# Optimization experiments

Measured on AMD Instinct MI355X. Metric: run time of the kernel, lower is better.

The kernel has to match this reference:

```python
import jax, jax.numpy as jnp
import numpy as np

VOCAB = 50265
HIDDEN = 768
NUM_LABELS = 2
B, S = 2, 4096


def setup_inputs() -> dict:
    key = jax.random.key(0)
    k1, k2, k3, k4 = jax.random.split(key, 4)
    # near-one-hot / soft distribution over vocab per token (positive values)
    embedding = jax.random.uniform(k1, (B, S, VOCAB), dtype=jnp.float32)
    attention_masks = jnp.ones((B, S), dtype=jnp.int32)
    # nn.Linear(vocab, hidden, bias=False): weight shape (hidden, vocab)
    W_embed = jax.random.normal(k2, (HIDDEN, VOCAB), dtype=jnp.float32) * 0.02
    token_mask = jnp.ones((VOCAB,), dtype=jnp.float32)
    W_cls = jax.random.normal(k3, (NUM_LABELS, HIDDEN), dtype=jnp.float32) * 0.02
    b_cls = jax.random.normal(k4, (NUM_LABELS,), dtype=jnp.float32) * 0.02
    return {"embedding": embedding, "attention_masks": attention_masks,
            "W_embed": W_embed, "token_mask": token_mask,
            "W_cls": W_cls, "b_cls": b_cls}


def reference(embedding, attention_masks, W_embed, token_mask, W_cls, b_cls):
    # norm_data=True: normalize each token's vocab distribution to sum 1
    normalized = embedding / jnp.sum(embedding, axis=-1, keepdims=True)
    # masked one-hot -> dense GEMM with embedding weight: (B,S,V) @ (V,H)
    emb = jnp.einsum('bsv,hv->bsh', normalized * token_mask, W_embed)
    # NOTE: pretrained Longformer body (self.bert) is an external pretrained
    # module; the kernel-relevant math (one-hot GEMM + classifier head) is
    # reproduced here. Classifier applied to the hidden states.
    logits = jnp.einsum('bsh,lh->bsl', emb, W_cls) + b_cls
    return logits
```

## Files before the change

### kernel.cpp

```cpp
#include <hip/hip_runtime.h>
#include <stdint.h>

typedef float vfloat4 __attribute__((ext_vector_type(4)));

constexpr int CHUNK = 4096;
constexpr int TG    = 16;
constexpr int VT    = 2048;
constexpr int MAXNG = 24;

__global__ __launch_bounds__(256) void fuse_partial_kernel(
    const float* __restrict__ Wemb,
    const float* __restrict__ Wcls,
    float* __restrict__ part,
    const int V, const int Vp, const int H, const int NG, const int NVT)
{
    __shared__ float sW0[1024];
    __shared__ float sW1[1024];
    for (int i = threadIdx.x; i < H; i += 256) { sW0[i] = Wcls[i]; sW1[i] = Wcls[H + i]; }
    __syncthreads();

    const int vt = blockIdx.x % NVT;
    const int g  = blockIdx.x / NVT;
    const int HS = (H + NG - 1) / NG;
    const int h0 = g * HS;
    const int h1 = min(H, h0 + HS);
    const int v  = vt * VT + (int)threadIdx.x * 8;

    float a0[8], a1[8];
    #pragma unroll
    for (int k = 0; k < 8; ++k) { a0[k] = 0.f; a1[k] = 0.f; }

    if (v + 8 <= V) {
        for (int h = h0; h < h1; ++h) {
            const float* p = Wemb + (size_t)h * (size_t)V + v;
            vfloat4 x0, x1;
            __builtin_memcpy(&x0, p,     16);
            __builtin_memcpy(&x1, p + 4, 16);
            const float w0 = sW0[h], w1 = sW1[h];
            a0[0] = fmaf(w0, x0.x, a0[0]);
            a0[1] = fmaf(w0, x0.y, a0[1]);
            a0[2] = fmaf(w0, x0.z, a0[2]);
            a0[3] = fmaf(w0, x0.w, a0[3]);
            a0[4] = fmaf(w0, x1.x, a0[4]);
            a0[5] = fmaf(w0, x1.y, a0[5]);
            a0[6] = fmaf(w0, x1.z, a0[6]);
            a0[7] = fmaf(w0, x1.w, a0[7]);
            a1[0] = fmaf(w1, x0.x, a1[0]);
            a1[1] = fmaf(w1, x0.y, a1[1]);
            a1[2] = fmaf(w1, x0.z, a1[2]);
            a1[3] = fmaf(w1, x0.w, a1[3]);
            a1[4] = fmaf(w1, x1.x, a1[4]);
            a1[5] = fmaf(w1, x1.y, a1[5]);
            a1[6] = fmaf(w1, x1.z, a1[6]);
            a1[7] = fmaf(w1, x1.w, a1[7]);
        }
        float* p0 = part + (size_t)g * 2 * (size_t)Vp + v;
        float* p1 = p0 + Vp;
        vfloat4 s00 = {a0[0], a0[1], a0[2], a0[3]};
        vfloat4 s01 = {a0[4], a0[5], a0[6], a0[7]};
        vfloat4 s10 = {a1[0], a1[1], a1[2], a1[3]};
        vfloat4 s11 = {a1[4], a1[5], a1[6], a1[7]};
        *(vfloat4*)(p0)     = s00;
        *(vfloat4*)(p0 + 4) = s01;
        *(vfloat4*)(p1)     = s10;
        *(vfloat4*)(p1 + 4) = s11;
    } else if (v < V) {
        for (int h = h0; h < h1; ++h) {
            const float w0 = sW0[h], w1 = sW1[h];
            const float* p = Wemb + (size_t)h * (size_t)V;
            #pragma unroll
            for (int k = 0; k < 8; ++k) {
                if (v + k < V) {
                    float x = p[v + k];
                    a0[k] = fmaf(w0, x, a0[k]);
                    a1[k] = fmaf(w1, x, a1[k]);
                }
            }
        }
        float* p0 = part + (size_t)g * 2 * (size_t)Vp;
        #pragma unroll
        for (int k = 0; k < 8; ++k) {
            if (v + k < V) { p0[v + k] = a0[k]; p0[Vp + v + k] = a1[k]; }
        }
    }
}

__global__ __launch_bounds__(256) void fuse_reduce_kernel(
    const float* __restrict__ part,
    const float* __restrict__ tmask,
    float2* __restrict__ wf2,
    const int V, const int Vp, const int NG)
{
    const int v = blockIdx.x * 256 + threadIdx.x;
    if (v >= V) return;
    float s0 = 0.f, s1 = 0.f;
    for (int g = 0; g < NG; ++g) {
        const float* p0 = part + (size_t)g * 2 * (size_t)Vp;
        s0 += p0[v];
        s1 += p0[Vp + v];
    }
    const float m = tmask[v];
    wf2[v] = make_float2(s0 * m, s1 * m);
}

__global__ __launch_bounds__(256) void fuse_weights_kernel(
    const float* __restrict__ Wemb,
    const float* __restrict__ tmask,
    const float* __restrict__ Wcls,
    float2* __restrict__ wf2,
    int V, int H)
{
    __shared__ float sW0[1024];
    __shared__ float sW1[1024];
    __shared__ float part[4][64][2];

    for (int i = threadIdx.x; i < H; i += blockDim.x) {
        sW0[i] = Wcls[i];
        sW1[i] = Wcls[H + i];
    }
    __syncthreads();

    const int vl = threadIdx.x & 63;
    const int hg = threadIdx.x >> 6;
    const int v  = blockIdx.x * 64 + vl;

    float a0 = 0.f, a1 = 0.f;
    if (v < V) {
        for (int h = hg; h < H; h += 4) {
            float w = Wemb[(size_t)h * (size_t)V + v];
            a0 = fmaf(w, sW0[h], a0);
            a1 = fmaf(w, sW1[h], a1);
        }
    }
    part[hg][vl][0] = a0;
    part[hg][vl][1] = a1;
    __syncthreads();

    if (hg == 0 && v < V) {
        float r0 = (part[0][vl][0] + part[1][vl][0]) + (part[2][vl][0] + part[3][vl][0]);
        float r1 = (part[0][vl][1] + part[1][vl][1]) + (part[2][vl][1] + part[3][vl][1]);
        float m = tmask[v];
        wf2[v] = make_float2(r0 * m, r1 * m);
    }
}

__global__ __launch_bounds__(256) void partial_kernel(
    const float* __restrict__ emb,
    const float2* __restrict__ wf2,
    float4* __restrict__ part,
    const int V, const int T, const int NC)
{
    __shared__ float lw0[CHUNK];
    __shared__ float lw1[CHUNK];
    __shared__ float red[4][TG][3];

    const int c    = blockIdx.x % NC;
    const int g    = blockIdx.x / NC;
    const int v0   = c * CHUNK;
    const int clen = min(CHUNK, V - v0);
    const int tid  = threadIdx.x;

    for (int i = tid; i < clen; i += 256) {
        float2 w = wf2[v0 + i];
        lw0[i] = w.x;
        lw1[i] = w.y;
    }
    __syncthreads();

    const int t0 = g * TG;
    float sA[TG], dA0[TG], dA1[TG];

    if (clen == CHUNK) {
        #pragma unroll
        for (int tk = 0; tk < TG; ++tk) {
            const float* rp = emb + (size_t)(t0 + tk) * (size_t)V + v0;
            float s = 0.f, d0 = 0.f, d1 = 0.f;
            #pragma unroll
            for (int jj = 0; jj < CHUNK / 1024; ++jj) {
                const int v4 = (tid + jj * 256) << 2;
                vfloat4 ev;
                __builtin_memcpy(&ev, rp + v4, 16);
                const vfloat4 w0 = *(const vfloat4*)(lw0 + v4);
                const vfloat4 w1 = *(const vfloat4*)(lw1 + v4);
                s += (ev.x + ev.y) + (ev.z + ev.w);
                d0 = fmaf(ev.x, w0.x, d0);
                d0 = fmaf(ev.y, w0.y, d0);
                d0 = fmaf(ev.z, w0.z, d0);
                d0 = fmaf(ev.w, w0.w, d0);
                d1 = fmaf(ev.x, w1.x, d1);
                d1 = fmaf(ev.y, w1.y, d1);
                d1 = fmaf(ev.z, w1.z, d1);
                d1 = fmaf(ev.w, w1.w, d1);
            }
            sA[tk] = s; dA0[tk] = d0; dA1[tk] = d1;
        }
    } else {
        const int nb4 = clen >> 2;
        const int rem = clen & 3;
        #pragma unroll
        for (int tk = 0; tk < TG; ++tk) {
            const float* rp = emb + (size_t)(t0 + tk) * (size_t)V + v0;
            float s = 0.f, d0 = 0.f, d1 = 0.f;
            for (int j = tid; j < nb4; j += 256) {
                const int v4 = j << 2;
                vfloat4 ev;
                __builtin_memcpy(&ev, rp + v4, 16);
                const vfloat4 w0 = *(const vfloat4*)(lw0 + v4);
                const vfloat4 w1 = *(const vfloat4*)(lw1 + v4);
                s += (ev.x + ev.y) + (ev.z + ev.w);
                d0 = fmaf(ev.x, w0.x, d0);
                d0 = fmaf(ev.y, w0.y, d0);
                d0 = fmaf(ev.z, w0.z, d0);
                d0 = fmaf(ev.w, w0.w, d0);
                d1 = fmaf(ev.x, w1.x, d1);
                d1 = fmaf(ev.y, w1.y, d1);
                d1 = fmaf(ev.z, w1.z, d1);
                d1 = fmaf(ev.w, w1.w, d1);
            }
            if (tid < rem) {
                const int v = (nb4 << 2) + tid;
                float e = rp[v];
                s += e;
                d0 = fmaf(e, lw0[v], d0);
                d1 = fmaf(e, lw1[v], d1);
            }
            sA[tk] = s; dA0[tk] = d0; dA1[tk] = d1;
        }
    }

    #pragma unroll
    for (int tk = 0; tk < TG; ++tk) {
        float s = sA[tk], d0 = dA0[tk], d1 = dA1[tk];
        #pragma unroll
        for (int off = 32; off > 0; off >>= 1) {
            s  += __shfl_xor(s,  off);
            d0 += __shfl_xor(d0, off);
            d1 += __shfl_xor(d1, off);
        }
        if ((tid & 63) == 0) {
            const int w = tid >> 6;
            red[w][tk][0] = s; red[w][tk][1] = d0; red[w][tk][2] = d1;
        }
    }
    __syncthreads();

    if (tid < TG) {
        float S  = (red[0][tid][0] + red[1][tid][0]) + (red[2][tid][0] + red[3][tid][0]);
        float D0 = (red[0][tid][1] + red[1][tid][1]) + (red[2][tid][1] + red[3][tid][1]);
        float D1 = (red[0][tid][2] + red[1][tid][2]) + (red[2][tid][2] + red[3][tid][2]);
        part[(size_t)c * T + (t0 + tid)] = make_float4(S, D0, D1, 0.f);
    }
}

__global__ __launch_bounds__(256) void finalize_kernel(
    const float4* __restrict__ part,
    const float* __restrict__ bcls,
    float2* __restrict__ out,
    const int T, const int NC)
{
    const int t = blockIdx.x * 256 + threadIdx.x;
    if (t >= T) return;
    float S = 0.f, D0 = 0.f, D1 = 0.f;
    for (int c = 0; c < NC; ++c) {
        float4 p = part[(size_t)c * T + t];
        S += p.x; D0 += p.y; D1 += p.z;
    }
    out[t] = make_float2(D0 / S + bcls[0], D1 / S + bcls[1]);
}

extern "C" void kernel_launch(void* const* d_in, const int* in_sizes, int n_in,
                              void* d_out, int out_size, void* d_ws, size_t ws_size,
                              hipStream_t stream) {
    const float* emb   = (const float*)d_in[0];
    const float* Wemb  = (const float*)d_in[2];
    const float* tmask = (const float*)d_in[3];
    const float* Wcls  = (const float*)d_in[4];
    const float* bcls  = (const float*)d_in[5];

    const int V  = in_sizes[3];
    const int T  = in_sizes[1];
    const int H  = in_sizes[2] / V;
    const int NC = (V + CHUNK - 1) / CHUNK;
    const int Vp = (V + 7) & ~7;

    float2* wf2 = (float2*)d_ws;
    const size_t wf2_b   = (((size_t)V * 8) + 255) & ~(size_t)255;
    const size_t k2p_b   = (((size_t)NC * T * 16) + 255) & ~(size_t)255;
    float4* k2part = (float4*)((char*)d_ws + wf2_b);
    const size_t off_k1p = wf2_b + k2p_b;
    float*  k1part = (float*)((char*)d_ws + off_k1p);

    const size_t per_g = (size_t)2 * Vp * 4;
    int NG = 0;
    if (ws_size > off_k1p) NG = (int)((ws_size - off_k1p) / per_g);
    if (NG > MAXNG) NG = MAXNG;

    if (NG >= 2) {
        const int NVT = (V + VT - 1) / VT;
        fuse_partial_kernel<<<NVT * NG, 256, 0, stream>>>(Wemb, Wcls, k1part, V, Vp, H, NG, NVT);
        fuse_reduce_kernel<<<(V + 255) / 256, 256, 0, stream>>>(k1part, tmask, wf2, V, Vp, NG);
    } else {
        const int blocks1 = (V + 63) / 64;
        fuse_weights_kernel<<<blocks1, 256, 0, stream>>>(Wemb, tmask, Wcls, wf2, V, H);
    }

    const int blocks2 = NC * (T / TG);
    partial_kernel<<<blocks2, 256, 0, stream>>>(emb, wf2, k2part, V, T, NC);

    const int blocks3 = (T + 255) / 256;
    finalize_kernel<<<blocks3, 256, 0, stream>>>(k2part, bcls, (float2*)d_out, T, NC);
}
```

Before: 377.4 us.

## Align token-row loads per residue and keep fused weights in registers

The partial kernel now assigns each block tokens sharing the same row alignment residue (t mod 4). It shifts the chunk start by a per-residue offset so the 16-byte loads of each embedding row are aligned, and handles the few leading elements separately. The fused classifier weights are loaded straight into registers instead of staged through LDS, which drops the shared-memory fill and its barrier. The first fuse kernel also switches from 8 contiguous floats per thread to a 256-stride coalesced pattern. The cost is more index arithmetic and a more complex tail path, with the tail now reading weights from global memory.

```diff
diff --git a/kernel.cpp b/kernel.cpp
--- a/kernel.cpp
+++ b/kernel.cpp
@@ -24,63 +24,45 @@
     const int HS = (H + NG - 1) / NG;
     const int h0 = g * HS;
     const int h1 = min(H, h0 + HS);
-    const int v  = vt * VT + (int)threadIdx.x * 8;
+    const int base = vt * VT + (int)threadIdx.x;
 
     float a0[8], a1[8];
     #pragma unroll
-    for (int k = 0; k < 8; ++k) { a0[k] = 0.f; a1[k] = 0.f; }
-
-    if (v + 8 <= V) {
+    for (int j = 0; j < 8; ++j) { a0[j] = 0.f; a1[j] = 0.f; }
+
+    if ((vt + 1) * VT <= V) {
         for (int h = h0; h < h1; ++h) {
-            const float* p = Wemb + (size_t)h * (size_t)V + v;
-            vfloat4 x0, x1;
-            __builtin_memcpy(&x0, p,     16);
-            __builtin_memcpy(&x1, p + 4, 16);
+            const float* p = Wemb + (size_t)h * (size_t)V + base;
             const float w0 = sW0[h], w1 = sW1[h];
-            a0[0] = fmaf(w0, x0.x, a0[0]);
-            a0[1] = fmaf(w0, x0.y, a0[1]);
-            a0[2] = fmaf(w0, x0.z, a0[2]);
-            a0[3] = fmaf(w0, x0.w, a0[3]);
-            a0[4] = fmaf(w0, x1.x, a0[4]);
-            a0[5] = fmaf(w0, x1.y, a0[5]);
-            a0[6] = fmaf(w0, x1.z, a0[6]);
-            a0[7] = fmaf(w0, x1.w, a0[7]);
-            a1[0] = fmaf(w1, x0.x, a1[0]);
-            a1[1] = fmaf(w1, x0.y, a1[1]);
-            a1[2] = fmaf(w1, x0.z, a1[2]);
-            a1[3] = fmaf(w1, x0.w, a1[3]);
-            a1[4] = fmaf(w1, x1.x, a1[4]);
-            a1[5] = fmaf(w1, x1.y, a1[5]);
-            a1[6] = fmaf(w1, x1.z, a1[6]);
-            a1[7] = fmaf(w1, x1.w, a1[7]);
-        }
-        float* p0 = part + (size_t)g * 2 * (size_t)Vp + v;
-        float* p1 = p0 + Vp;
-        vfloat4 s00 = {a0[0], a0[1], a0[2], a0[3]};
-        vfloat4 s01 = {a0[4], a0[5], a0[6], a0[7]};
-        vfloat4 s10 = {a1[0], a1[1], a1[2], a1[3]};
-        vfloat4 s11 = {a1[4], a1[5], a1[6], a1[7]};
-        *(vfloat4*)(p0)     = s00;
-        *(vfloat4*)(p0 + 4) = s01;
-        *(vfloat4*)(p1)     = s10;
-        *(vfloat4*)(p1 + 4) = s11;
-    } else if (v < V) {
+            #pragma unroll
+            for (int j = 0; j < 8; ++j) {
+                float x = p[j * 256];
+                a0[j] = fmaf(w0, x, a0[j]);
+                a1[j] = fmaf(w1, x, a1[j]);
+            }
+        }
+        float* o0 = part + (size_t)g * 2 * (size_t)Vp + base;
+        #pragma unroll
+        for (int j = 0; j < 8; ++j) { o0[j * 256] = a0[j]; o0[Vp + j * 256] = a1[j]; }
+    } else {
         for (int h = h0; h < h1; ++h) {
+            const float* p = Wemb + (size_t)h * (size_t)V;
             const float w0 = sW0[h], w1 = sW1[h];
-            const float* p = Wemb + (size_t)h * (size_t)V;
-            #pragma unroll
-            for (int k = 0; k < 8; ++k) {
-                if (v + k < V) {
-                    float x = p[v + k];
-                    a0[k] = fmaf(w0, x, a0[k]);
-                    a1[k] = fmaf(w1, x, a1[k]);
+            #pragma unroll
+            for (int j = 0; j < 8; ++j) {
+                const int v = base + j * 256;
+                if (v < V) {
+                    float x = p[v];
+                    a0[j] = fmaf(w0, x, a0[j]);
+                    a1[j] = fmaf(w1, x, a1[j]);
                 }
             }
         }
-        float* p0 = part + (size_t)g * 2 * (size_t)Vp;
+        float* o0 = part + (size_t)g * 2 * (size_t)Vp;
         #pragma unroll
-        for (int k = 0; k < 8; ++k) {
-            if (v + k < V) { p0[v + k] = a0[k]; p0[Vp + v + k] = a1[k]; }
+        for (int j = 0; j < 8; ++j) {
+            const int v = base + j * 256;
+            if (v < V) { o0[v] = a0[j]; o0[Vp + v] = a1[j]; }
         }
     }
 }
@@ -104,11 +86,8 @@
 }
 
 __global__ __launch_bounds__(256) void fuse_weights_kernel(
-    const float* __restrict__ Wemb,
-    const float* __restrict__ tmask,
-    const float* __restrict__ Wcls,
-    float2* __restrict__ wf2,
-    int V, int H)
+    const float* __restrict__ Wemb, const float* __restrict__ tmask,
+    const float* __restrict__ Wcls, float2* __restrict__ wf2, int V, int H)
 {
     __shared__ float sW0[1024];
     __shared__ float sW1[1024];
@@ -150,113 +129,114 @@
     float4* __restrict__ part,
     const int V, const int T, const int NC)
 {
-    __shared__ float lw0[CHUNK];
-    __shared__ float lw1[CHUNK];
     __shared__ float red[4][TG][3];
 
-    const int c    = blockIdx.x % NC;
-    const int g    = blockIdx.x / NC;
-    const int v0   = c * CHUNK;
-    const int clen = min(CHUNK, V - v0);
-    const int tid  = threadIdx.x;
-
-    for (int i = tid; i < clen; i += 256) {
-        float2 w = wf2[v0 + i];
-        lw0[i] = w.x;
-        lw1[i] = w.y;
-    }
-    __syncthreads();
-
-    const int t0 = g * TG;
-    float sA[TG], dA0[TG], dA1[TG];
-
-    if (clen == CHUNK) {
+    const int tid = threadIdx.x;
+    const int c   = blockIdx.x % NC;
+    const int g   = blockIdx.x / NC;
+    const int r   = g & 3;
+    const int q   = g >> 2;
+    const int h   = (4 - r) & 3;
+    const int wstart = h + c * CHUNK;
+    const int wlen   = min(CHUNK, V - wstart);
+    const int voff   = tid << 2;
+    const int wv     = tid >> 6;
+
+    if (wlen == CHUNK) {
+        vfloat4 w0v[4], w1v[4];
         #pragma unroll
+        for (int jj = 0; jj < 4; ++jj) {
+            float2 f[4];
+            __builtin_memcpy(f, wf2 + (wstart + voff + jj * 1024), 32);
+            w0v[jj] = (vfloat4){f[0].x, f[1].x, f[2].x, f[3].x};
+            w1v[jj] = (vfloat4){f[0].y, f[1].y, f[2].y, f[3].y};
+        }
+
         for (int tk = 0; tk < TG; ++tk) {
-            const float* rp = emb + (size_t)(t0 + tk) * (size_t)V + v0;
+            const int t = r + 64 * q + 4 * tk;
+            const float* rp = emb + (size_t)t * (size_t)V + wstart;
             float s = 0.f, d0 = 0.f, d1 = 0.f;
             #pragma unroll
-            for (int jj = 0; jj < CHUNK / 1024; ++jj) {
-                const int v4 = (tid + jj * 256) << 2;
-                vfloat4 ev;
-                __builtin_memcpy(&ev, rp + v4, 16);
-                const vfloat4 w0 = *(const vfloat4*)(lw0 + v4);
-                const vfloat4 w1 = *(const vfloat4*)(lw1 + v4);
+            for (int jj = 0; jj < 4; ++jj) {
+                const vfloat4 ev = *(const vfloat4*)(rp + voff + jj * 1024);
                 s += (ev.x + ev.y) + (ev.z + ev.w);
-                d0 = fmaf(ev.x, w0.x, d0);
-                d0 = fmaf(ev.y, w0.y, d0);
-                d0 = fmaf(ev.z, w0.z, d0);
-                d0 = fmaf(ev.w, w0.w, d0);
-                d1 = fmaf(ev.x, w1.x, d1);
-                d1 = fmaf(ev.y, w1.y, d1);
-                d1 = fmaf(ev.z, w1.z, d1);
-                d1 = fmaf(ev.w, w1.w, d1);
-            }
-            sA[tk] = s; dA0[tk] = d0; dA1[tk] = d1;
+                d0 = fmaf(ev.x, w0v[jj].x, d0);
+                d0 = fmaf(ev.y, w0v[jj].y, d0);
+                d0 = fmaf(ev.z, w0v[jj].z, d0);
+                d0 = fmaf(ev.w, w0v[jj].w, d0);
+                d1 = fmaf(ev.x, w1v[jj].x, d1);
+                d1 = fmaf(ev.y, w1v[jj].y, d1);
+                d1 = fmaf(ev.z, w1v[jj].z, d1);
+                d1 = fmaf(ev.w, w1v[jj].w, d1);
+            }
+            if (c == 0 && tid < h) {
+                const float e = emb[(size_t)t * (size_t)V + tid];
+                const float2 w = wf2[tid];
+                s += e; d0 = fmaf(e, w.x, d0); d1 = fmaf(e, w.y, d1);
+            }
+            #pragma unroll
+            for (int off = 32; off > 0; off >>= 1) {
+                s  += __shfl_xor(s,  off);
+                d0 += __shfl_xor(d0, off);
+                d1 += __shfl_xor(d1, off);
+            }
+            if ((tid & 63) == 0) {
+                red[wv][tk][0] = s; red[wv][tk][1] = d0; red[wv][tk][2] = d1;
+            }
         }
     } else {
-        const int nb4 = clen >> 2;
-        const int rem = clen & 3;
-        #pragma unroll
+        const int nb4 = wlen >> 2;
+        const int rem = wlen & 3;
         for (int tk = 0; tk < TG; ++tk) {
-            const float* rp = emb + (size_t)(t0 + tk) * (size_t)V + v0;
+            const int t = r + 64 * q + 4 * tk;
+            const float* rp = emb + (size_t)t * (size_t)V + wstart;
             float s = 0.f, d0 = 0.f, d1 = 0.f;
             for (int j = tid; j < nb4; j += 256) {
                 const int v4 = j << 2;
-                vfloat4 ev;
-                __builtin_memcpy(&ev, rp + v4, 16);
-                const vfloat4 w0 = *(const vfloat4*)(lw0 + v4);
-                const vfloat4 w1 = *(const vfloat4*)(lw1 + v4);
+                const vfloat4 ev = *(const vfloat4*)(rp + v4);
+                float2 f[4];
+                __builtin_memcpy(f, wf2 + (wstart + v4), 32);
                 s += (ev.x + ev.y) + (ev.z + ev.w);
-                d0 = fmaf(ev.x, w0.x, d0);
-                d0 = fmaf(ev.y, w0.y, d0);
-                d0 = fmaf(ev.z, w0.z, d0);
-                d0 = fmaf(ev.w, w0.w, d0);
-                d1 = fmaf(ev.x, w1.x, d1);
-                d1 = fmaf(ev.y, w1.y, d1);
-                d1 = fmaf(ev.z, w1.z, d1);
-                d1 = fmaf(ev.w, w1.w, d1);
+                d0 = fmaf(ev.x, f[0].x, d0);
+                d0 = fmaf(ev.y, f[1].x, d0);
+                d0 = fmaf(ev.z, f[2].x, d0);
+                d0 = fmaf(ev.w, f[3].x, d0);
+                d1 = fmaf(ev.x, f[0].y, d1);
+                d1 = fmaf(ev.y, f[1].y, d1);
+                d1 = fmaf(ev.z, f[2].y, d1);
+                d1 = fmaf(ev.w, f[3].y, d1);
             }
             if (tid < rem) {
                 const int v = (nb4 << 2) + tid;
-                float e = rp[v];
-                s += e;
-                d0 = fmaf(e, lw0[v], d0);
-                d1 = fmaf(e, lw1[v], d1);
-            }
-            sA[tk] = s; dA0[tk] = d0; dA1[tk] = d1;
-        }
-    }
-
-    #pragma unroll
-    for (int tk = 0; tk < TG; ++tk) {
-        float s = sA[tk], d0 = dA0[tk], d1 = dA1[tk];
-        #pragma unroll
-        for (int off = 32; off > 0; off >>= 1) {
-            s  += __shfl_xor(s,  off);
-            d0 += __shfl_xor(d0, off);
-            d1 += __shfl_xor(d1, off);
-        }
-        if ((tid & 63) == 0) {
-            const int w = tid >> 6;
-            red[w][tk][0] = s; red[w][tk][1] = d0; red[w][tk][2] = d1;
+                const float e = rp[v];
+                const float2 w = wf2[wstart + v];
+                s += e; d0 = fmaf(e, w.x, d0); d1 = fmaf(e, w.y, d1);
+            }
+            #pragma unroll
+            for (int off = 32; off > 0; off >>= 1) {
+                s  += __shfl_xor(s,  off);
+                d0 += __shfl_xor(d0, off);
+                d1 += __shfl_xor(d1, off);
+            }
+            if ((tid & 63) == 0) {
+                red[wv][tk][0] = s; red[wv][tk][1] = d0; red[wv][tk][2] = d1;
+            }
         }
     }
     __syncthreads();
 
     if (tid < TG) {
-        float S  = (red[0][tid][0] + red[1][tid][0]) + (red[2][tid][0] + red[3][tid][0]);
-        float D0 = (red[0][tid][1] + red[1][tid][1]) + (red[2][tid][1] + red[3][tid][1]);
-        float D1 = (red[0][tid][2] + red[1][tid][2]) + (red[2][tid][2] + red[3][tid][2]);
-        part[(size_t)c * T + (t0 + tid)] = make_float4(S, D0, D1, 0.f);
+        const float S  = (red[0][tid][0] + red[1][tid][0]) + (red[2][tid][0] + red[3][tid][0]);
+        const float D0 = (red[0][tid][1] + red[1][tid][1]) + (red[2][tid][1] + red[3][tid][1]);
+        const float D1 = (red[0][tid][2] + red[1][tid][2]) + (red[2][tid][2] + red[3][tid][2]);
+        const int t = r + 64 * q + 4 * tid;
+        part[(size_t)c * T + t] = make_float4(S, D0, D1, 0.f);
     }
 }
 
 __global__ __launch_bounds__(256) void finalize_kernel(
-    const float4* __restrict__ part,
-    const float* __restrict__ bcls,
-    float2* __restrict__ out,
-    const int T, const int NC)
+    const float4* __restrict__ part, const float* __restrict__ bcls,
+    float2* __restrict__ out, const int T, const int NC)
 {
     const int t = blockIdx.x * 256 + threadIdx.x;
     if (t >= T) return;
@@ -300,13 +280,11 @@
         fuse_partial_kernel<<<NVT * NG, 256, 0, stream>>>(Wemb, Wcls, k1part, V, Vp, H, NG, NVT);
         fuse_reduce_kernel<<<(V + 255) / 256, 256, 0, stream>>>(k1part, tmask, wf2, V, Vp, NG);
     } else {
-        const int blocks1 = (V + 63) / 64;
-        fuse_weights_kernel<<<blocks1, 256, 0, stream>>>(Wemb, tmask, Wcls, wf2, V, H);
+        fuse_weights_kernel<<<(V + 63) / 64, 256, 0, stream>>>(Wemb, tmask, Wcls, wf2, V, H);
     }
 
     const int blocks2 = NC * (T / TG);
     partial_kernel<<<blocks2, 256, 0, stream>>>(emb, wf2, k2part, V, T, NC);
 
-    const int blocks3 = (T + 255) / 256;
-    finalize_kernel<<<blocks3, 256, 0, stream>>>(k2part, bcls, (float2*)d_out, T, NC);
-}
+    finalize_kernel<<<(T + 255) / 256, 256, 0, stream>>>(k2part, bcls, (float2*)d_out, T, NC);
+}
```

Result: no change. 383.7 us (+1.7%).
